# Optimization experiments

Measured on AMD Instinct MI355X. Metric: run time of the kernel, lower is better.

The kernel has to match this reference:

```python
import jax, jax.numpy as jnp
import numpy as np

N = 100000
E = 600000
HID = 128
L = 2
BN_EPS = 1e-5


def setup_inputs() -> dict:
    key = jax.random.key(0)
    ks = jax.random.split(key, 20)
    s = 0.05
    inp = {
        "x": jax.random.normal(ks[0], (N, 128), jnp.float32),
        "edge_index": jax.random.randint(ks[1], (2, E), 0, N, jnp.int64 if jax.config.jax_enable_x64 else jnp.int32),
        "edge_attr": jax.random.normal(ks[2], (E, 1), jnp.float32),
        # backbone params
        "lin_W": jax.random.normal(ks[3], (128, HID), jnp.float32) * s,
        "lin_b": jnp.zeros((HID,), jnp.float32),
        "enc_W": jax.random.normal(ks[4], (1, HID), jnp.float32) * s,
        "enc_b": jnp.zeros((HID,), jnp.float32),
        # per-layer GIN params, stacked over L layers
        "eps": jnp.zeros((L,), jnp.float32),
        "e1_W": jax.random.normal(ks[5], (L, 1, HID), jnp.float32) * s,
        "e1_b": jnp.zeros((L, HID), jnp.float32),
        "e2_W": jax.random.normal(ks[6], (L, HID, HID), jnp.float32) * s,
        "e2_b": jnp.zeros((L, HID), jnp.float32),
        "m1_W": jax.random.normal(ks[7], (L, HID, 2 * HID), jnp.float32) * s,
        "m1_b": jnp.zeros((L, 2 * HID), jnp.float32),
        "bn_g": jnp.ones((L, 2 * HID), jnp.float32),
        "bn_b": jnp.zeros((L, 2 * HID), jnp.float32),
        "m2_W": jax.random.normal(ks[8], (L, 2 * HID, HID), jnp.float32) * s,
        "m2_b": jnp.zeros((L, HID), jnp.float32),
    }
    return inp


def _gin_layer(h, src, dst, edge_attr, eps, e1_W, e1_b, e2_W, e2_b,
               m1_W, m1_b, bn_g, bn_b, m2_W, m2_b):
    # edge encoder: Linear(1,H) -> ReLU -> Linear(H,H)
    ee = jax.nn.relu(edge_attr @ e1_W + e1_b) @ e2_W + e2_b      # [E,H]
    msg = jax.nn.relu(h[src] + ee)                               # gather + relu
    agg = jax.ops.segment_sum(msg, dst, num_segments=h.shape[0])  # scatter-add
    z = (1.0 + eps) * h + agg
    z = z @ m1_W + m1_b                                          # [N,2H]
    mu = jnp.mean(z, axis=0)
    var = jnp.mean((z - mu) ** 2, axis=0)                        # biased (train-mode BN)
    z = (z - mu) * jax.lax.rsqrt(var + BN_EPS) * bn_g + bn_b
    z = jax.nn.relu(z)
    return z @ m2_W + m2_b                                       # [N,H]


def reference(x, edge_index, edge_attr, lin_W, lin_b, enc_W, enc_b, eps,
              e1_W, e1_b, e2_W, e2_b, m1_W, m1_b, bn_g, bn_b, m2_W, m2_b):
    src, dst = edge_index[0], edge_index[1]
    # in_dim > 1 -> linear projection path
    h = x @ lin_W + lin_b                                        # [N,H]
    ee0 = edge_attr @ enc_W + enc_b                              # [E,H]
    new_h = h.at[src].set(jax.nn.relu(h[src] + ee0))
    new_h = new_h.at[dst].set(jax.nn.relu(h[dst] + ee0))
    h = new_h
    for l in range(L):
        h = _gin_layer(h, src, dst, edge_attr, eps[l], e1_W[l], e1_b[l],
                       e2_W[l], e2_b[l], m1_W[l], m1_b[l], bn_g[l], bn_b[l],
                       m2_W[l], m2_b[l])
        if l < L - 1:
            h = jax.nn.relu(h)
        # dropout omitted for determinism
    return h
```

## Files before the change

kernel.cpp:

```cpp
#include <hip/hip_runtime.h>

#define N_NODES 100000
#define E_EDGES 600000
#define HID 128

typedef __attribute__((ext_vector_type(8))) short short8v;
typedef __attribute__((ext_vector_type(4))) float f32x4;

__device__ __forceinline__ unsigned short bf16rne(float x) {
  unsigned u = __float_as_uint(x);
  return (unsigned short)((u + 0x7FFFu + ((u >> 16) & 1u)) >> 16);
}
__device__ __forceinline__ float bf16tof(unsigned short u) {
  return __uint_as_float(((unsigned)u) << 16);
}

__global__ void k_last(const int* __restrict__ ei, int* __restrict__ last_src,
                       int* __restrict__ last_dst, int* __restrict__ deg, int E) {
  int e = blockIdx.x * blockDim.x + threadIdx.x;
  if (e >= E) return;
  int s = ei[e], d = ei[E + e];
  atomicMax(&last_src[s], e);
  atomicMax(&last_dst[d], e);
  atomicAdd(&deg[d], 1);
}

__global__ __launch_bounds__(256) void k_scan1(const int* __restrict__ deg,
                                               int* __restrict__ excl,
                                               int* __restrict__ bsum, int n) {
  __shared__ int sh[256];
  int b = blockIdx.x, t = threadIdx.x;
  int i0 = b * 1024 + t * 4;
  int v0 = (i0 + 0 < n) ? deg[i0 + 0] : 0;
  int v1 = (i0 + 1 < n) ? deg[i0 + 1] : 0;
  int v2 = (i0 + 2 < n) ? deg[i0 + 2] : 0;
  int v3 = (i0 + 3 < n) ? deg[i0 + 3] : 0;
  int tsum = v0 + v1 + v2 + v3;
  sh[t] = tsum;
  __syncthreads();
  for (int off = 1; off < 256; off <<= 1) {
    int add = (t >= off) ? sh[t - off] : 0;
    __syncthreads();
    sh[t] += add;
    __syncthreads();
  }
  int ex = sh[t] - tsum;
  if (i0 + 0 < n) excl[i0 + 0] = ex;
  if (i0 + 1 < n) excl[i0 + 1] = ex + v0;
  if (i0 + 2 < n) excl[i0 + 2] = ex + v0 + v1;
  if (i0 + 3 < n) excl[i0 + 3] = ex + v0 + v1 + v2;
  if (t == 255) bsum[b] = sh[255];
}

__global__ void k_scan2(const int* __restrict__ bsum, int* __restrict__ boff, int nb) {
  __shared__ int sh[128];
  int t = threadIdx.x;
  int v = (t < nb) ? bsum[t] : 0;
  sh[t] = v;
  __syncthreads();
  for (int off = 1; off < 128; off <<= 1) {
    int add = (t >= off) ? sh[t - off] : 0;
    __syncthreads();
    sh[t] += add;
    __syncthreads();
  }
  if (t < nb) boff[t] = sh[t] - v;
}

__global__ void k_scatter(const int* __restrict__ ei, const float* __restrict__ ea,
                          const int* __restrict__ excl, const int* __restrict__ boff,
                          int* __restrict__ cnt, int* __restrict__ swv,
                          float* __restrict__ awv, int E) {
  int e = blockIdx.x * blockDim.x + threadIdx.x;
  if (e >= E) return;
  int d = ei[E + e];
  int p = excl[d] + boff[d >> 10] + atomicAdd(&cnt[d], 1);
  swv[p] = ei[e];
  awv[p] = ea[e];
}

__global__ void k_table(const float* __restrict__ W1g, const float* __restrict__ b1g,
                        const float* __restrict__ W2g, const float* __restrict__ b2g,
                        float* __restrict__ tabA, float* __restrict__ tabB,
                        float* __restrict__ tsort) {
  __shared__ float w1[128], b1[128], key[128];
  __shared__ int idx[128];
  __shared__ float w2[128][128];
  const int t = threadIdx.x;
  w1[t] = W1g[t];
  b1[t] = b1g[t];
  for (int k = 0; k < 128; ++k) w2[k][t] = W2g[k * 128 + t];
  __syncthreads();
  float s0 = w1[t];
  key[t] = (s0 != 0.0f) ? (-b1[t] / s0) : __builtin_inff();
  idx[t] = t;
  for (int size = 2; size <= 128; size <<= 1) {
    for (int stride = size >> 1; stride > 0; stride >>= 1) {
      __syncthreads();
      int p = t ^ stride;
      if (p > t) {
        bool up = ((t & size) == 0);
        float k1 = key[t], k2 = key[p];
        if (up == (k1 > k2)) {
          int i1 = idx[t], i2 = idx[p];
          key[t] = k2; key[p] = k1; idx[t] = i2; idx[p] = i1;
        }
      }
    }
  }
  __syncthreads();
  tsort[t] = key[t];
  float A = 0.0f, B = b2g[t];
  for (int k = 0; k < 128; ++k) {
    float s = w1[k], bb = b1[k], w = w2[k][t];
    if (s < 0.0f) { A = fmaf(s, w, A); B = fmaf(bb, w, B); }
    else if (s == 0.0f && bb > 0.0f) { B = fmaf(bb, w, B); }
  }
  tabA[t] = A;
  tabB[t] = B;
  for (int i = 0; i < 128; ++i) {
    float kv = key[i];
    int kk = idx[i];
    if (kv < __builtin_inff()) {
      float s = w1[kk], bb = b1[kk], w = w2[kk][t];
      if (s > 0.0f) { A = fmaf(s, w, A); B = fmaf(bb, w, B); }
      else { A = fmaf(-s, w, A); B = fmaf(-bb, w, B); }
    }
    tabA[(i + 1) * 128 + t] = A;
    tabB[(i + 1) * 128 + t] = B;
  }
}

__global__ __launch_bounds__(256) void k_pos(const int* __restrict__ swv,
                                             const float* __restrict__ awv,
                                             const float* __restrict__ tsort,
                                             int* __restrict__ spk, int E) {
  __shared__ float ts[128];
  if (threadIdx.x < 128) ts[threadIdx.x] = tsort[threadIdx.x];
  __syncthreads();
  int i = blockIdx.x * blockDim.x + threadIdx.x;
  if (i >= E) return;
  float a = awv[i];
  int pos = 0;
#pragma unroll
  for (int st = 64; st > 0; st >>= 1)
    if (pos + st <= 128 && ts[pos + st - 1] < a) pos += st;
  spk[i] = swv[i] | (pos << 20);
}

__global__ __launch_bounds__(256) void k_agg(
    const float* __restrict__ h, const int* __restrict__ spk,
    const float* __restrict__ awv, const int* __restrict__ excl,
    const int* __restrict__ boff, const float* __restrict__ tabA,
    const float* __restrict__ tabB, const float* __restrict__ epsP,
    unsigned* __restrict__ zin, int N, int E) {
  int w = __builtin_amdgcn_readfirstlane((int)((blockIdx.x * 256 + threadIdx.x) >> 6));
  if (w >= N) return;
  int lane = threadIdx.x & 63;
  int start = excl[w] + boff[w >> 10];
  int end = (w + 1 < N) ? (excl[w + 1] + boff[(w + 1) >> 10]) : E;
  int j = lane * 2;
  float a0 = 0.0f, a1 = 0.0f, c0 = 0.0f, c1 = 0.0f;
  int i = start;
  for (; i + 2 <= end; i += 2) {
    int sp0 = spk[i], sp1 = spk[i + 1];
    float aa = awv[i], ab = awv[i + 1];
    int s0 = sp0 & 0xFFFFF, p0 = sp0 >> 20;
    int s1 = sp1 & 0xFFFFF, p1 = sp1 >> 20;
    float2 h0 = *(const float2*)(h + (size_t)s0 * HID + j);
    float2 A0 = *(const float2*)(tabA + (size_t)p0 * HID + j);
    float2 B0 = *(const float2*)(tabB + (size_t)p0 * HID + j);
    float2 h1 = *(const float2*)(h + (size_t)s1 * HID + j);
    float2 A1 = *(const float2*)(tabA + (size_t)p1 * HID + j);
    float2 B1 = *(const float2*)(tabB + (size_t)p1 * HID + j);
    a0 += fmaxf(h0.x + fmaf(A0.x, aa, B0.x), 0.0f);
    a1 += fmaxf(h0.y + fmaf(A0.y, aa, B0.y), 0.0f);
    c0 += fmaxf(h1.x + fmaf(A1.x, ab, B1.x), 0.0f);
    c1 += fmaxf(h1.y + fmaf(A1.y, ab, B1.y), 0.0f);
  }
  if (i < end) {
    int sp0 = spk[i];
    float aa = awv[i];
    int s0 = sp0 & 0xFFFFF, p0 = sp0 >> 20;
    float2 h0 = *(const float2*)(h + (size_t)s0 * HID + j);
    float2 A0 = *(const float2*)(tabA + (size_t)p0 * HID + j);
    float2 B0 = *(const float2*)(tabB + (size_t)p0 * HID + j);
    a0 += fmaxf(h0.x + fmaf(A0.x, aa, B0.x), 0.0f);
    a1 += fmaxf(h0.y + fmaf(A0.y, aa, B0.y), 0.0f);
  }
  a0 += c0;
  a1 += c1;
  float ep1 = 1.0f + *epsP;
  float2 hn = *(const float2*)(h + (size_t)w * HID + j);
  float ox = fmaf(ep1, hn.x, a0);
  float oy = fmaf(ep1, hn.y, a1);
  zin[(size_t)w * 64 + lane] = (unsigned)bf16rne(ox) | ((unsigned)bf16rne(oy) << 16);
}

__device__ __forceinline__ void pack_one(const float* __restrict__ W, int K, int M,
                                         int t, unsigned short* __restrict__ out) {
  int lane = t & 63, f = t >> 6;
  int KS = K >> 5;
  int mt = f / KS, ks = f - mt * KS;
  int col = mt * 16 + (lane & 15);
  int kb = ks * 32 + ((lane >> 4) * 8);
  unsigned r0, r1, r2, r3;
  r0 = bf16rne(W[(size_t)(kb + 0) * M + col]) | ((unsigned)bf16rne(W[(size_t)(kb + 1) * M + col]) << 16);
  r1 = bf16rne(W[(size_t)(kb + 2) * M + col]) | ((unsigned)bf16rne(W[(size_t)(kb + 3) * M + col]) << 16);
  r2 = bf16rne(W[(size_t)(kb + 4) * M + col]) | ((unsigned)bf16rne(W[(size_t)(kb + 5) * M + col]) << 16);
  r3 = bf16rne(W[(size_t)(kb + 6) * M + col]) | ((unsigned)bf16rne(W[(size_t)(kb + 7) * M + col]) << 16);
  uint4 v = make_uint4(r0, r1, r2, r3);
  *(uint4*)(out + ((size_t)f * 64 + lane) * 8) = v;
}

__global__ __launch_bounds__(256) void k_pack(
    const float* __restrict__ lin_W, const float* __restrict__ m1_W,
    const float* __restrict__ m2_W, unsigned short* __restrict__ pk_lin,
    unsigned short* __restrict__ pk_m1, unsigned short* __restrict__ pk_m2) {
  int t = blockIdx.x * 256 + threadIdx.x;
  if (t < 2048) {
    pack_one(lin_W, 128, 128, t, pk_lin);
  } else if (t < 10240) {
    int u = t - 2048;
    int l = u >> 12;
    pack_one(m1_W + (size_t)l * 128 * 256, 128, 256, u & 4095, pk_m1 + (size_t)l * 32768);
  } else if (t < 18432) {
    int u = t - 10240;
    int l = u >> 12;
    pack_one(m2_W + (size_t)l * 256 * 128, 256, 128, u & 4095, pk_m2 + (size_t)l * 32768);
  }
}

template <int K, int M, int MODE, bool RELU_OUT>
__global__ __launch_bounds__(256) void k_mgemm(
    const void* __restrict__ in0, const unsigned short* __restrict__ pkW,
    const float* __restrict__ bias, void* __restrict__ outv,
    const float* __restrict__ pre_a, const float* __restrict__ pre_b,
    float* __restrict__ pS1, float* __restrict__ pS2,
    const int* __restrict__ last_dst, const int* __restrict__ last_src,
    const float* __restrict__ ea, const float* __restrict__ encW,
    const float* __restrict__ encb) {
  constexpr int KS = K / 32, MT = M / 16;
  __shared__ float red[(MODE == 1) ? 2048 : 1];
  const int t = threadIdx.x;
  const int w = t >> 6, lane = t & 63;
  const int row0 = blockIdx.x * 64 + w * 16;
  const int arow = row0 + (lane & 15);
  const int rg = arow < N_NODES ? arow : N_NODES - 1;
  const int kb = (lane >> 4) * 8;

  short8v afrag[KS];
#pragma unroll
  for (int ks = 0; ks < KS; ++ks) {
    const int k0 = ks * 32 + kb;
    if (MODE == 0) {
      const float* in = (const float*)in0;
      float4 v0 = *(const float4*)(in + (size_t)rg * K + k0);
      float4 v1 = *(const float4*)(in + (size_t)rg * K + k0 + 4);
      short8v a;
      a[0] = (short)bf16rne(v0.x); a[1] = (short)bf16rne(v0.y);
      a[2] = (short)bf16rne(v0.z); a[3] = (short)bf16rne(v0.w);
      a[4] = (short)bf16rne(v1.x); a[5] = (short)bf16rne(v1.y);
      a[6] = (short)bf16rne(v1.z); a[7] = (short)bf16rne(v1.w);
      afrag[ks] = a;
    } else if (MODE == 1) {
      afrag[ks] = *(const short8v*)((const unsigned short*)in0 + (size_t)rg * K + k0);
    } else {
      short8v raw = *(const short8v*)((const unsigned short*)in0 + (size_t)rg * K + k0);
      float4 sa0 = *(const float4*)(pre_a + k0);
      float4 sa1 = *(const float4*)(pre_a + k0 + 4);
      float4 sb0 = *(const float4*)(pre_b + k0);
      float4 sb1 = *(const float4*)(pre_b + k0 + 4);
      short8v a;
      a[0] = (short)bf16rne(fmaxf(fmaf(bf16tof((unsigned short)raw[0]), sa0.x, sb0.x), 0.0f));
      a[1] = (short)bf16rne(fmaxf(fmaf(bf16tof((unsigned short)raw[1]), sa0.y, sb0.y), 0.0f));
      a[2] = (short)bf16rne(fmaxf(fmaf(bf16tof((unsigned short)raw[2]), sa0.z, sb0.z), 0.0f));
      a[3] = (short)bf16rne(fmaxf(fmaf(bf16tof((unsigned short)raw[3]), sa0.w, sb0.w), 0.0f));
      a[4] = (short)bf16rne(fmaxf(fmaf(bf16tof((unsigned short)raw[4]), sa1.x, sb1.x), 0.0f));
      a[5] = (short)bf16rne(fmaxf(fmaf(bf16tof((unsigned short)raw[5]), sa1.y, sb1.y), 0.0f));
      a[6] = (short)bf16rne(fmaxf(fmaf(bf16tof((unsigned short)raw[6]), sa1.z, sb1.z), 0.0f));
      a[7] = (short)bf16rne(fmaxf(fmaf(bf16tof((unsigned short)raw[7]), sa1.w, sb1.w), 0.0f));
      afrag[ks] = a;
    }
  }

  f32x4 acc[MT];
#pragma unroll
  for (int mt = 0; mt < MT; ++mt) acc[mt] = (f32x4){0.f, 0.f, 0.f, 0.f};
#pragma unroll
  for (int mt = 0; mt < MT; ++mt) {
#pragma unroll
    for (int ks = 0; ks < KS; ++ks) {
      short8v bfrag = *(const short8v*)(pkW + ((size_t)(mt * KS + ks) * 64 + lane) * 8);
      acc[mt] = __builtin_amdgcn_mfma_f32_16x16x32_bf16(afrag[ks], bfrag, acc[mt], 0, 0, 0);
    }
  }

  const int colb = lane & 15;
  const int rbase = row0 + (lane >> 4) * 4;
#pragma unroll
  for (int mt = 0; mt < MT; ++mt) {
    const int col = mt * 16 + colb;
    const float b = bias[col];
    if (MODE == 1) {
      unsigned short* out = (unsigned short*)outv;
      float s1 = 0.0f, s2 = 0.0f;
#pragma unroll
      for (int r = 0; r < 4; ++r) {
        int R = rbase + r;
        if (R < N_NODES) {
          float v = acc[mt][r] + b;
          out[(size_t)R * M + col] = bf16rne(v);
          s1 += v;
          s2 = fmaf(v, v, s2);
        }
      }
      s1 += __shfl_xor(s1, 16);
      s1 += __shfl_xor(s1, 32);
      s2 += __shfl_xor(s2, 16);
      s2 += __shfl_xor(s2, 32);
      if (lane < 16) {
        red[w * 256 + col] = s1;
        red[1024 + w * 256 + col] = s2;
      }
    } else if (MODE == 2) {
      float* out = (float*)outv;
#pragma unroll
      for (int r = 0; r < 4; ++r) {
        int R = rbase + r;
        if (R < N_NODES) {
          float v = acc[mt][r] + b;
          if (RELU_OUT) v = fmaxf(v, 0.0f);
          out[(size_t)R * M + col] = v;
        }
      }
    } else {
      float* out = (float*)outv;
      const float ew = encW[col], eb = encb[col];
#pragma unroll
      for (int r = 0; r < 4; ++r) {
        int R = rbase + r;
        if (R < N_NODES) {
          float v = acc[mt][r] + b;
          int ld = last_dst[R];
          int ls = last_src[R];
          int e = (ld >= 0) ? ld : ls;
          if (e >= 0) v = fmaxf(v + fmaf(ea[e], ew, eb), 0.0f);
          out[(size_t)R * M + col] = v;
        }
      }
    }
  }
  if (MODE == 1) {
    __syncthreads();
    if (t < 256) {
      float a = red[t] + red[256 + t] + red[512 + t] + red[768 + t];
      float q = red[1024 + t] + red[1280 + t] + red[1536 + t] + red[1792 + t];
      pS1[(size_t)blockIdx.x * 256 + t] = a;
      pS2[(size_t)blockIdx.x * 256 + t] = q;
    }
  }
}

__global__ __launch_bounds__(256) void k_bnred(
    const float* __restrict__ pS1, const float* __restrict__ pS2,
    float* __restrict__ qS1, float* __restrict__ qS2, int nblk) {
  int j = threadIdx.x;
  int b = blockIdx.x;
  float s1 = 0.0f, s2 = 0.0f;
  for (int i = b; i < nblk; i += 64) {
    s1 += pS1[(size_t)i * 256 + j];
    s2 += pS2[(size_t)i * 256 + j];
  }
  qS1[b * 256 + j] = s1;
  qS2[b * 256 + j] = s2;
}

__global__ __launch_bounds__(256) void k_bnfin2(
    const float* __restrict__ qS1, const float* __restrict__ qS2,
    const float* __restrict__ g, const float* __restrict__ bb,
    float* __restrict__ scale, float* __restrict__ shift) {
  int j = threadIdx.x;
  float s1 = 0.0f, s2 = 0.0f;
#pragma unroll 8
  for (int i = 0; i < 64; ++i) {
    s1 += qS1[i * 256 + j];
    s2 += qS2[i * 256 + j];
  }
  const float inv = 1.0f / (float)N_NODES;
  float mu = s1 * inv;
  float var = s2 * inv - mu * mu;
  float sc = g[j] * rsqrtf(var + 1e-5f);
  scale[j] = sc;
  shift[j] = fmaf(-mu, sc, bb[j]);
}

extern "C" void kernel_launch(void* const* d_in, const int* in_sizes, int n_in,
                              void* d_out, int out_size, void* d_ws, size_t ws_size,
                              hipStream_t stream) {
  const float* x     = (const float*)d_in[0];
  const int*   ei    = (const int*)d_in[1];
  const float* ea    = (const float*)d_in[2];
  const float* lin_W = (const float*)d_in[3];
  const float* lin_b = (const float*)d_in[4];
  const float* enc_W = (const float*)d_in[5];
  const float* enc_b = (const float*)d_in[6];
  const float* eps   = (const float*)d_in[7];
  const float* e1_W  = (const float*)d_in[8];
  const float* e1_b  = (const float*)d_in[9];
  const float* e2_W  = (const float*)d_in[10];
  const float* e2_b  = (const float*)d_in[11];
  const float* m1_W  = (const float*)d_in[12];
  const float* m1_b  = (const float*)d_in[13];
  const float* bn_g  = (const float*)d_in[14];
  const float* bn_b  = (const float*)d_in[15];
  const float* m2_W  = (const float*)d_in[16];
  const float* m2_b  = (const float*)d_in[17];
  float* hbuf = (float*)d_out;

  const int NB_SCAN = (N_NODES + 1023) / 1024;
  const int NB_GEMM = (N_NODES + 63) / 64;

  float* ws = (float*)d_ws;
  size_t o = 0;
  unsigned* zin_u = (unsigned*)(ws + o);          o += (size_t)N_NODES * 64;
  unsigned short* z2_u = (unsigned short*)(ws + o); o += (size_t)N_NODES * 128;
  int* last_dst = (int*)(ws + o);  o += N_NODES;
  int* last_src = (int*)(ws + o);  o += N_NODES;
  int* deg = (int*)(ws + o);       o += N_NODES;
  int* cnt = (int*)(ws + o);       o += N_NODES;
  int* excl = (int*)(ws + o);      o += N_NODES;
  int* bsum = (int*)(ws + o);      o += 128;
  int* boff = (int*)(ws + o);      o += 128;
  int* swv = (int*)(ws + o);       o += E_EDGES;
  float* awv = ws + o;             o += E_EDGES;
  int* spk = (int*)(ws + o);       o += E_EDGES;
  float* tabA = ws + o;            o += 129 * 128;
  float* tabB = ws + o;            o += 129 * 128;
  float* tsort = ws + o;           o += 128;
  float* pS1 = ws + o;             o += (size_t)NB_GEMM * 256;
  float* pS2 = ws + o;             o += (size_t)NB_GEMM * 256;
  float* qS1 = ws + o;             o += 64 * 256;
  float* qS2 = ws + o;             o += 64 * 256;
  float* scale = ws + o;           o += 256;
  float* shift = ws + o;           o += 256;
  unsigned short* pk_lin = (unsigned short*)(ws + o); o += 8192;
  unsigned short* pk_m1  = (unsigned short*)(ws + o); o += 32768;
  unsigned short* pk_m2  = (unsigned short*)(ws + o); o += 32768;
  if (ws_size < o * sizeof(float)) return;

  hipMemsetAsync(last_dst, 0xFF, 2 * (size_t)N_NODES * sizeof(int), stream);
  hipMemsetAsync(deg, 0, 2 * (size_t)N_NODES * sizeof(int), stream);
  k_last<<<(E_EDGES + 255) / 256, 256, 0, stream>>>(ei, last_src, last_dst, deg, E_EDGES);
  k_scan1<<<NB_SCAN, 256, 0, stream>>>(deg, excl, bsum, N_NODES);
  k_scan2<<<1, 128, 0, stream>>>(bsum, boff, NB_SCAN);
  k_scatter<<<(E_EDGES + 255) / 256, 256, 0, stream>>>(ei, ea, excl, boff, cnt, swv, awv, E_EDGES);
  k_pack<<<72, 256, 0, stream>>>(lin_W, m1_W, m2_W, pk_lin, pk_m1, pk_m2);

  k_mgemm<128, 128, 0, false><<<NB_GEMM, 256, 0, stream>>>(
      x, pk_lin, lin_b, hbuf, nullptr, nullptr, nullptr, nullptr,
      last_dst, last_src, ea, enc_W, enc_b);

  for (int l = 0; l < 2; ++l) {
    k_table<<<1, 128, 0, stream>>>(e1_W + l * 128, e1_b + l * 128,
                                   e2_W + l * 128 * 128, e2_b + l * 128,
                                   tabA, tabB, tsort);
    k_pos<<<(E_EDGES + 255) / 256, 256, 0, stream>>>(swv, awv, tsort, spk, E_EDGES);
    k_agg<<<(N_NODES * 64 + 255) / 256, 256, 0, stream>>>(
        hbuf, spk, awv, excl, boff, tabA, tabB, eps + l, zin_u, N_NODES, E_EDGES);
    k_mgemm<128, 256, 1, false><<<NB_GEMM, 256, 0, stream>>>(
        zin_u, pk_m1 + (size_t)l * 32768, m1_b + l * 256, z2_u, nullptr, nullptr,
        pS1, pS2, nullptr, nullptr, nullptr, nullptr, nullptr);
    k_bnred<<<64, 256, 0, stream>>>(pS1, pS2, qS1, qS2, NB_GEMM);
    k_bnfin2<<<1, 256, 0, stream>>>(qS1, qS2, bn_g + l * 256, bn_b + l * 256,
                                    scale, shift);
    if (l == 0) {
      k_mgemm<256, 128, 2, true><<<NB_GEMM, 256, 0, stream>>>(
          z2_u, pk_m2 + (size_t)l * 32768, m2_b + l * 128, hbuf, scale, shift,
          nullptr, nullptr, nullptr, nullptr, nullptr, nullptr, nullptr);
    } else {
      k_mgemm<256, 128, 2, false><<<NB_GEMM, 256, 0, stream>>>(
          z2_u, pk_m2 + (size_t)l * 32768, m2_b + l * 128, hbuf, scale, shift,
          nullptr, nullptr, nullptr, nullptr, nullptr, nullptr, nullptr);
    }
  }
}
```

Baseline: 686.9 us.

## Store hidden state in bf16, pack edge pairs, precompute both layers' tables once

Intermediate node features are now kept in a bf16 workspace buffer, which halves the bytes read by the gather in the aggregation kernel. Source index and edge attribute are packed into one int2 per sorted edge, and the per-edge position into the piecewise table is stored as a byte per layer. The table and position kernels now run once for both layers instead of once per layer. The cost is extra bf16 rounding of the hidden state, which may add numerical error.

```diff
diff --git a/kernel.cpp b/kernel.cpp
--- a/kernel.cpp
+++ b/kernel.cpp
@@ -69,20 +69,26 @@
 
 __global__ void k_scatter(const int* __restrict__ ei, const float* __restrict__ ea,
                           const int* __restrict__ excl, const int* __restrict__ boff,
-                          int* __restrict__ cnt, int* __restrict__ swv,
-                          float* __restrict__ awv, int E) {
+                          int* __restrict__ cnt, int2* __restrict__ pairE, int E) {
   int e = blockIdx.x * blockDim.x + threadIdx.x;
   if (e >= E) return;
   int d = ei[E + e];
   int p = excl[d] + boff[d >> 10] + atomicAdd(&cnt[d], 1);
-  swv[p] = ei[e];
-  awv[p] = ea[e];
-}
-
-__global__ void k_table(const float* __restrict__ W1g, const float* __restrict__ b1g,
-                        const float* __restrict__ W2g, const float* __restrict__ b2g,
+  pairE[p] = make_int2(ei[e], __float_as_int(ea[e]));
+}
+
+__global__ void k_table(const float* __restrict__ e1_W, const float* __restrict__ e1_b,
+                        const float* __restrict__ e2_W, const float* __restrict__ e2_b,
                         float* __restrict__ tabA, float* __restrict__ tabB,
                         float* __restrict__ tsort) {
+  const int l = blockIdx.x;
+  const float* W1g = e1_W + l * 128;
+  const float* b1g = e1_b + l * 128;
+  const float* W2g = e2_W + l * 128 * 128;
+  const float* b2g = e2_b + l * 128;
+  float* tA = tabA + (size_t)l * 129 * 128;
+  float* tB = tabB + (size_t)l * 129 * 128;
+  float* tS = tsort + l * 128;
   __shared__ float w1[128], b1[128], key[128];
   __shared__ int idx[128];
   __shared__ float w2[128][128];
@@ -109,15 +115,15 @@
     }
   }
   __syncthreads();
-  tsort[t] = key[t];
+  tS[t] = key[t];
   float A = 0.0f, B = b2g[t];
   for (int k = 0; k < 128; ++k) {
     float s = w1[k], bb = b1[k], w = w2[k][t];
     if (s < 0.0f) { A = fmaf(s, w, A); B = fmaf(bb, w, B); }
     else if (s == 0.0f && bb > 0.0f) { B = fmaf(bb, w, B); }
   }
-  tabA[t] = A;
-  tabB[t] = B;
+  tA[t] = A;
+  tB[t] = B;
   for (int i = 0; i < 128; ++i) {
     float kv = key[i];
     int kk = idx[i];
@@ -126,31 +132,37 @@
       if (s > 0.0f) { A = fmaf(s, w, A); B = fmaf(bb, w, B); }
       else { A = fmaf(-s, w, A); B = fmaf(-bb, w, B); }
     }
-    tabA[(i + 1) * 128 + t] = A;
-    tabB[(i + 1) * 128 + t] = B;
-  }
-}
-
-__global__ __launch_bounds__(256) void k_pos(const int* __restrict__ swv,
-                                             const float* __restrict__ awv,
+    tA[(i + 1) * 128 + t] = A;
+    tB[(i + 1) * 128 + t] = B;
+  }
+}
+
+__global__ __launch_bounds__(256) void k_pos(const int2* __restrict__ pairE,
                                              const float* __restrict__ tsort,
-                                             int* __restrict__ spk, int E) {
-  __shared__ float ts[128];
-  if (threadIdx.x < 128) ts[threadIdx.x] = tsort[threadIdx.x];
+                                             unsigned char* __restrict__ posb0,
+                                             unsigned char* __restrict__ posb1, int E) {
+  __shared__ float ts0[128], ts1[128];
+  if (threadIdx.x < 128) {
+    ts0[threadIdx.x] = tsort[threadIdx.x];
+    ts1[threadIdx.x] = tsort[128 + threadIdx.x];
+  }
   __syncthreads();
   int i = blockIdx.x * blockDim.x + threadIdx.x;
   if (i >= E) return;
-  float a = awv[i];
-  int pos = 0;
-#pragma unroll
-  for (int st = 64; st > 0; st >>= 1)
-    if (pos + st <= 128 && ts[pos + st - 1] < a) pos += st;
-  spk[i] = swv[i] | (pos << 20);
+  float a = __int_as_float(pairE[i].y);
+  int p0 = 0, p1 = 0;
+#pragma unroll
+  for (int st = 64; st > 0; st >>= 1) {
+    if (p0 + st <= 128 && ts0[p0 + st - 1] < a) p0 += st;
+    if (p1 + st <= 128 && ts1[p1 + st - 1] < a) p1 += st;
+  }
+  posb0[i] = (unsigned char)p0;
+  posb1[i] = (unsigned char)p1;
 }
 
 __global__ __launch_bounds__(256) void k_agg(
-    const float* __restrict__ h, const int* __restrict__ spk,
-    const float* __restrict__ awv, const int* __restrict__ excl,
+    const unsigned short* __restrict__ h, const int2* __restrict__ pairE,
+    const unsigned char* __restrict__ posb, const int* __restrict__ excl,
     const int* __restrict__ boff, const float* __restrict__ tabA,
     const float* __restrict__ tabB, const float* __restrict__ epsP,
     unsigned* __restrict__ zin, int N, int E) {
@@ -163,37 +175,36 @@
   float a0 = 0.0f, a1 = 0.0f, c0 = 0.0f, c1 = 0.0f;
   int i = start;
   for (; i + 2 <= end; i += 2) {
-    int sp0 = spk[i], sp1 = spk[i + 1];
-    float aa = awv[i], ab = awv[i + 1];
-    int s0 = sp0 & 0xFFFFF, p0 = sp0 >> 20;
-    int s1 = sp1 & 0xFFFFF, p1 = sp1 >> 20;
-    float2 h0 = *(const float2*)(h + (size_t)s0 * HID + j);
+    int2 pr0 = pairE[i], pr1 = pairE[i + 1];
+    int p0 = posb[i], p1 = posb[i + 1];
+    float aa = __int_as_float(pr0.y), ab = __int_as_float(pr1.y);
+    unsigned hv0 = *(const unsigned*)(h + (size_t)pr0.x * HID + j);
     float2 A0 = *(const float2*)(tabA + (size_t)p0 * HID + j);
     float2 B0 = *(const float2*)(tabB + (size_t)p0 * HID + j);
-    float2 h1 = *(const float2*)(h + (size_t)s1 * HID + j);
+    unsigned hv1 = *(const unsigned*)(h + (size_t)pr1.x * HID + j);
     float2 A1 = *(const float2*)(tabA + (size_t)p1 * HID + j);
     float2 B1 = *(const float2*)(tabB + (size_t)p1 * HID + j);
-    a0 += fmaxf(h0.x + fmaf(A0.x, aa, B0.x), 0.0f);
-    a1 += fmaxf(h0.y + fmaf(A0.y, aa, B0.y), 0.0f);
-    c0 += fmaxf(h1.x + fmaf(A1.x, ab, B1.x), 0.0f);
-    c1 += fmaxf(h1.y + fmaf(A1.y, ab, B1.y), 0.0f);
+    a0 += fmaxf(__uint_as_float(hv0 << 16) + fmaf(A0.x, aa, B0.x), 0.0f);
+    a1 += fmaxf(__uint_as_float(hv0 & 0xFFFF0000u) + fmaf(A0.y, aa, B0.y), 0.0f);
+    c0 += fmaxf(__uint_as_float(hv1 << 16) + fmaf(A1.x, ab, B1.x), 0.0f);
+    c1 += fmaxf(__uint_as_float(hv1 & 0xFFFF0000u) + fmaf(A1.y, ab, B1.y), 0.0f);
   }
   if (i < end) {
-    int sp0 = spk[i];
-    float aa = awv[i];
-    int s0 = sp0 & 0xFFFFF, p0 = sp0 >> 20;
-    float2 h0 = *(const float2*)(h + (size_t)s0 * HID + j);
+    int2 pr0 = pairE[i];
+    int p0 = posb[i];
+    float aa = __int_as_float(pr0.y);
+    unsigned hv0 = *(const unsigned*)(h + (size_t)pr0.x * HID + j);
     float2 A0 = *(const float2*)(tabA + (size_t)p0 * HID + j);
     float2 B0 = *(const float2*)(tabB + (size_t)p0 * HID + j);
-    a0 += fmaxf(h0.x + fmaf(A0.x, aa, B0.x), 0.0f);
-    a1 += fmaxf(h0.y + fmaf(A0.y, aa, B0.y), 0.0f);
+    a0 += fmaxf(__uint_as_float(hv0 << 16) + fmaf(A0.x, aa, B0.x), 0.0f);
+    a1 += fmaxf(__uint_as_float(hv0 & 0xFFFF0000u) + fmaf(A0.y, aa, B0.y), 0.0f);
   }
   a0 += c0;
   a1 += c1;
   float ep1 = 1.0f + *epsP;
-  float2 hn = *(const float2*)(h + (size_t)w * HID + j);
-  float ox = fmaf(ep1, hn.x, a0);
-  float oy = fmaf(ep1, hn.y, a1);
+  unsigned hn = *(const unsigned*)(h + (size_t)w * HID + j);
+  float ox = fmaf(ep1, __uint_as_float(hn << 16), a0);
+  float oy = fmaf(ep1, __uint_as_float(hn & 0xFFFF0000u), a1);
   zin[(size_t)w * 64 + lane] = (unsigned)bf16rne(ox) | ((unsigned)bf16rne(oy) << 16);
 }
 
@@ -231,7 +242,7 @@
   }
 }
 
-template <int K, int M, int MODE, bool RELU_OUT>
+template <int K, int M, int MODE, bool RELU_OUT, bool OBF>
 __global__ __launch_bounds__(256) void k_mgemm(
     const void* __restrict__ in0, const unsigned short* __restrict__ pkW,
     const float* __restrict__ bias, void* __restrict__ outv,
@@ -324,18 +335,17 @@
         red[1024 + w * 256 + col] = s2;
       }
     } else if (MODE == 2) {
-      float* out = (float*)outv;
 #pragma unroll
       for (int r = 0; r < 4; ++r) {
         int R = rbase + r;
         if (R < N_NODES) {
           float v = acc[mt][r] + b;
           if (RELU_OUT) v = fmaxf(v, 0.0f);
-          out[(size_t)R * M + col] = v;
+          if (OBF) ((unsigned short*)outv)[(size_t)R * M + col] = bf16rne(v);
+          else ((float*)outv)[(size_t)R * M + col] = v;
         }
       }
     } else {
-      float* out = (float*)outv;
       const float ew = encW[col], eb = encb[col];
 #pragma unroll
       for (int r = 0; r < 4; ++r) {
@@ -346,7 +356,7 @@
           int ls = last_src[R];
           int e = (ld >= 0) ? ld : ls;
           if (e >= 0) v = fmaxf(v + fmaf(ea[e], ew, eb), 0.0f);
-          out[(size_t)R * M + col] = v;
+          ((unsigned short*)outv)[(size_t)R * M + col] = bf16rne(v);
         }
       }
     }
@@ -416,14 +426,14 @@
   const float* bn_b  = (const float*)d_in[15];
   const float* m2_W  = (const float*)d_in[16];
   const float* m2_b  = (const float*)d_in[17];
-  float* hbuf = (float*)d_out;
 
   const int NB_SCAN = (N_NODES + 1023) / 1024;
   const int NB_GEMM = (N_NODES + 63) / 64;
 
   float* ws = (float*)d_ws;
   size_t o = 0;
-  unsigned* zin_u = (unsigned*)(ws + o);          o += (size_t)N_NODES * 64;
+  unsigned short* hbuf = (unsigned short*)(ws + o); o += (size_t)N_NODES * 64;
+  unsigned* zin_u = (unsigned*)(ws + o);            o += (size_t)N_NODES * 64;
   unsigned short* z2_u = (unsigned short*)(ws + o); o += (size_t)N_NODES * 128;
   int* last_dst = (int*)(ws + o);  o += N_NODES;
   int* last_src = (int*)(ws + o);  o += N_NODES;
@@ -432,12 +442,12 @@
   int* excl = (int*)(ws + o);      o += N_NODES;
   int* bsum = (int*)(ws + o);      o += 128;
   int* boff = (int*)(ws + o);      o += 128;
-  int* swv = (int*)(ws + o);       o += E_EDGES;
-  float* awv = ws + o;             o += E_EDGES;
-  int* spk = (int*)(ws + o);       o += E_EDGES;
-  float* tabA = ws + o;            o += 129 * 128;
-  float* tabB = ws + o;            o += 129 * 128;
-  float* tsort = ws + o;           o += 128;
+  int2* pairE = (int2*)(ws + o);   o += (size_t)E_EDGES * 2;
+  unsigned char* posb0 = (unsigned char*)(ws + o); o += (E_EDGES + 3) / 4 + 4;
+  unsigned char* posb1 = (unsigned char*)(ws + o); o += (E_EDGES + 3) / 4 + 4;
+  float* tabA = ws + o;            o += 2 * 129 * 128;
+  float* tabB = ws + o;            o += 2 * 129 * 128;
+  float* tsort = ws + o;           o += 2 * 128;
   float* pS1 = ws + o;             o += (size_t)NB_GEMM * 256;
   float* pS2 = ws + o;             o += (size_t)NB_GEMM * 256;
   float* qS1 = ws + o;             o += 64 * 256;
@@ -451,36 +461,36 @@
 
   hipMemsetAsync(last_dst, 0xFF, 2 * (size_t)N_NODES * sizeof(int), stream);
   hipMemsetAsync(deg, 0, 2 * (size_t)N_NODES * sizeof(int), stream);
+  k_table<<<2, 128, 0, stream>>>(e1_W, e1_b, e2_W, e2_b, tabA, tabB, tsort);
   k_last<<<(E_EDGES + 255) / 256, 256, 0, stream>>>(ei, last_src, last_dst, deg, E_EDGES);
   k_scan1<<<NB_SCAN, 256, 0, stream>>>(deg, excl, bsum, N_NODES);
   k_scan2<<<1, 128, 0, stream>>>(bsum, boff, NB_SCAN);
-  k_scatter<<<(E_EDGES + 255) / 256, 256, 0, stream>>>(ei, ea, excl, boff, cnt, swv, awv, E_EDGES);
+  k_scatter<<<(E_EDGES + 255) / 256, 256, 0, stream>>>(ei, ea, excl, boff, cnt, pairE, E_EDGES);
+  k_pos<<<(E_EDGES + 255) / 256, 256, 0, stream>>>(pairE, tsort, posb0, posb1, E_EDGES);
   k_pack<<<72, 256, 0, stream>>>(lin_W, m1_W, m2_W, pk_lin, pk_m1, pk_m2);
 
-  k_mgemm<128, 128, 0, false><<<NB_GEMM, 256, 0, stream>>>(
+  k_mgemm<128, 128, 0, false, true><<<NB_GEMM, 256, 0, stream>>>(
       x, pk_lin, lin_b, hbuf, nullptr, nullptr, nullptr, nullptr,
       last_dst, last_src, ea, enc_W, enc_b);
 
   for (int l = 0; l < 2; ++l) {
-    k_table<<<1, 128, 0, stream>>>(e1_W + l * 128, e1_b + l * 128,
-                                   e2_W + l * 128 * 128, e2_b + l * 128,
-                                   tabA, tabB, tsort);
-    k_pos<<<(E_EDGES + 255) / 256, 256, 0, stream>>>(swv, awv, tsort, spk, E_EDGES);
     k_agg<<<(N_NODES * 64 + 255) / 256, 256, 0, stream>>>(
-        hbuf, spk, awv, excl, boff, tabA, tabB, eps + l, zin_u, N_NODES, E_EDGES);
-    k_mgemm<128, 256, 1, false><<<NB_GEMM, 256, 0, stream>>>(
+        hbuf, pairE, l == 0 ? posb0 : posb1, excl, boff,
+        tabA + (size_t)l * 129 * 128, tabB + (size_t)l * 129 * 128,
+        eps + l, zin_u, N_NODES, E_EDGES);
+    k_mgemm<128, 256, 1, false, true><<<NB_GEMM, 256, 0, stream>>>(
         zin_u, pk_m1 + (size_t)l * 32768, m1_b + l * 256, z2_u, nullptr, nullptr,
         pS1, pS2, nullptr, nullptr, nullptr, nullptr, nullptr);
     k_bnred<<<64, 256, 0, stream>>>(pS1, pS2, qS1, qS2, NB_GEMM);
     k_bnfin2<<<1, 256, 0, stream>>>(qS1, qS2, bn_g + l * 256, bn_b + l * 256,
                                     scale, shift);
     if (l == 0) {
-      k_mgemm<256, 128, 2, true><<<NB_GEMM, 256, 0, stream>>>(
-          z2_u, pk_m2 + (size_t)l * 32768, m2_b + l * 128, hbuf, scale, shift,
+      k_mgemm<256, 128, 2, true, true><<<NB_GEMM, 256, 0, stream>>>(
+          z2_u, pk_m2, m2_b, hbuf, scale, shift,
           nullptr, nullptr, nullptr, nullptr, nullptr, nullptr, nullptr);
     } else {
-      k_mgemm<256, 128, 2, false><<<NB_GEMM, 256, 0, stream>>>(
-          z2_u, pk_m2 + (size_t)l * 32768, m2_b + l * 128, hbuf, scale, shift,
+      k_mgemm<256, 128, 2, false, false><<<NB_GEMM, 256, 0, stream>>>(
+          z2_u, pk_m2 + 32768, m2_b + 128, d_out, scale, shift,
           nullptr, nullptr, nullptr, nullptr, nullptr, nullptr, nullptr);
     }
   }
```

Result: faster. 642.6 us (-6.4%).
